# Performance work log

Measured on AMD Instinct MI355X. Metric: run time of the kernel, lower is better.

The kernel has to match this reference:

```python
import jax, jax.numpy as jnp
import numpy as np

N, T, D, H = 4, 2048, 1024, 16
DH = D // H
NEG = -1e20


def setup_inputs() -> dict:
    key = jax.random.key(0)
    ks = jax.random.split(key, 6)
    std = 1.0 / np.sqrt(D)
    return {
        "query": jax.random.normal(ks[0], (N, T, D), jnp.float32),
        "mask": jax.random.randint(ks[1], (N, T), 0, 2, jnp.int32),
        "Wq": jax.random.normal(ks[2], (D, D), jnp.float32) * std,
        "bq": jnp.zeros((D,), jnp.float32),
        "Wk": jax.random.normal(ks[3], (D, D), jnp.float32) * std,
        "bk": jnp.zeros((D,), jnp.float32),
        "Wv": jax.random.normal(ks[4], (D, D), jnp.float32) * std,
        "bv": jnp.zeros((D,), jnp.float32),
        "Wo": jax.random.normal(ks[5], (D, D), jnp.float32) * std,
        "bo": jnp.zeros((D,), jnp.float32),
    }


def _heads(x):
    # [N,T,D] -> [N,H,T,DH]
    n, t, _ = x.shape
    return x.reshape(n, t, H, DH).transpose(0, 2, 1, 3)


def reference(query, mask, Wq, bq, Wk, bk, Wv, bv, Wo, bo):
    scale = jnp.asarray(np.sqrt(DH), query.dtype)
    q = _heads(query @ Wq.T + bq)
    k = _heads(query @ Wk.T + bk)  # self-attention: key = value = query
    v = _heads(query @ Wv.T + bv)
    dot = jnp.einsum("nhtd,nhsd->nhts", q, k)  # [N,H,T,T_k]
    # 2D mask [N,T] aligns by name to the QUERY axis: (N,1,T,1)
    attn_mask = (mask == 0)[:, None, :, None]
    dot = jnp.where(attn_mask, jnp.asarray(NEG, dot.dtype), dot)
    # faithful to source: scale applied AFTER masked_fill, inside softmax arg
    attn = jax.nn.softmax(dot / scale, axis=-1)
    ctx = jnp.einsum("nhts,nhsd->nhtd", attn, v)  # [N,H,T,DH]
    ctx = ctx.transpose(0, 2, 1, 3).reshape(query.shape[0], query.shape[1], D)
    return ctx @ Wo.T + bo
```

## Files before the change

kernel.cpp:

```cpp
#include <hip/hip_runtime.h>

typedef _Float16 f16;
typedef __attribute__((ext_vector_type(8))) _Float16 half8;
typedef __attribute__((ext_vector_type(4))) _Float16 half4;
typedef __attribute__((ext_vector_type(4))) float f32x4;
typedef __attribute__((ext_vector_type(16))) float f32x16;

#define DEVINL __device__ __forceinline__

constexpr int NBATCH = 4, T = 2048, D = 1024, H = 16, DH = 64;
constexpr int M = NBATCH * T;
constexpr float SCL2 = 0.18033688011f;

DEVINL void async16(const f16* g, f16* l) {
  __builtin_amdgcn_global_load_lds(
      (__attribute__((address_space(1))) void*)(g),
      (__attribute__((address_space(3))) void*)(l), 16, 0, 0);
}

DEVINL unsigned pk2(float x, float y) {
  auto h = __builtin_amdgcn_cvt_pkrtz(x, y);
  return __builtin_bit_cast(unsigned, h);
}

union H8U {
  half8 h;
  unsigned u[4];
};

__global__ void cvt_all_kernel(const float* __restrict__ query,
                               const float* __restrict__ wq, const float* __restrict__ wk,
                               const float* __restrict__ wv, const float* __restrict__ wo,
                               f16* __restrict__ dst) {
  constexpr int NQ4 = M * D / 4;
  constexpr int NW4 = D * D / 4;
  constexpr int NT4 = NQ4 + 4 * NW4;
  const float* srcs[4] = {wq, wk, wv, wo};
  int i = blockIdx.x * blockDim.x + threadIdx.x;
  int stride = gridDim.x * blockDim.x;
  for (; i < NT4; i += stride) {
    const float* s;
    int off;
    if (i < NQ4) { s = query; off = i; }
    else {
      int j = i - NQ4;
      s = srcs[j >> 18];
      off = j & (NW4 - 1);
    }
    float4 v = reinterpret_cast<const float4*>(s)[off];
    half4 h = {(f16)v.x, (f16)v.y, (f16)v.z, (f16)v.w};
    reinterpret_cast<half4*>(dst)[i] = h;
  }
}

template<bool F32OUT>
DEVINL void gemm_body(const f16* __restrict__ A, const f16* __restrict__ W,
                      const float* __restrict__ bias, void* __restrict__ out,
                      f16* As, f16* Bs, long bm, long bn, float oscale) {
  constexpr int K = 1024, BK = 32, NCOL = 1024;
  const int tid = threadIdx.x;
  const int lane = tid & 63, wave = tid >> 6;
  const int wr = wave >> 1, wc = wave & 1;
  const int srow = tid >> 2, scol = (tid & 3) * 8;
  const f16* gA = A + (bm + srow) * (long)K + scol;
  const f16* gB = W + (bn + srow) * (long)K + scol;
  f16* lA = &As[srow * BK + scol];
  f16* lB = &Bs[srow * BK + scol];
  const int fr = lane & 15, fk = (lane >> 4) * 8;
  f32x4 acc[4][4] = {};

  for (int k0 = 0; k0 < K; k0 += BK) {
    async16(gA + k0, lA);
    async16(gA + k0 + 64 * K, lA + 64 * BK);
    async16(gB + k0, lB);
    async16(gB + k0 + 64 * K, lB + 64 * BK);
    __syncthreads();
    half8 af[4], bf[4];
#pragma unroll
    for (int m = 0; m < 4; ++m)
      af[m] = *(const half8*)&As[(wr * 64 + m * 16 + fr) * BK + fk];
#pragma unroll
    for (int n = 0; n < 4; ++n)
      bf[n] = *(const half8*)&Bs[(wc * 64 + n * 16 + fr) * BK + fk];
#pragma unroll
    for (int m = 0; m < 4; ++m)
#pragma unroll
      for (int n = 0; n < 4; ++n)
        acc[m][n] = __builtin_amdgcn_mfma_f32_16x16x32_f16(af[m], bf[n], acc[m][n], 0, 0, 0);
    __syncthreads();
  }
  const int rq = (lane >> 4) * 4;
#pragma unroll
  for (int m = 0; m < 4; ++m) {
    const long row = bm + wr * 64 + m * 16 + rq;
#pragma unroll
    for (int n = 0; n < 4; ++n) {
      const long col = bn + wc * 64 + n * 16 + fr;
      const float bb = bias[col];
#pragma unroll
      for (int r = 0; r < 4; ++r) {
        float v = (acc[m][n][r] + bb) * oscale;
        if (F32OUT) ((float*)out)[(row + r) * (long)NCOL + col] = v;
        else        ((f16*)out)[(row + r) * (long)NCOL + col] = (f16)v;
      }
    }
  }
}

__global__ __launch_bounds__(256) void gemm_qkv(const f16* __restrict__ A,
                                                const f16* __restrict__ Wall,
                                                const float* __restrict__ bq,
                                                const float* __restrict__ bk,
                                                const float* __restrict__ bv,
                                                f16* __restrict__ Qh,
                                                f16* __restrict__ Kh,
                                                f16* __restrict__ Vh) {
  __shared__ __align__(16) f16 As[128 * 32];
  __shared__ __align__(16) f16 Bs[128 * 32];
  const int z = blockIdx.z;
  const f16* W = Wall + (size_t)z * D * D;
  const float* bias = z == 0 ? bq : (z == 1 ? bk : bv);
  f16* out = z == 0 ? Qh : (z == 1 ? Kh : Vh);
  const float oscale = z == 0 ? SCL2 : 1.0f;
  gemm_body<false>(A, W, bias, (void*)out, As, Bs,
                   (long)blockIdx.y * 128, (long)blockIdx.x * 128, oscale);
}

__global__ __launch_bounds__(256) void gemm_out(const f16* __restrict__ A,
                                                const f16* __restrict__ W,
                                                const float* __restrict__ bias,
                                                float* __restrict__ out) {
  __shared__ __align__(16) f16 As[128 * 32];
  __shared__ __align__(16) f16 Bs[128 * 32];
  gemm_body<true>(A, W, bias, (void*)out, As, Bs,
                  (long)blockIdx.y * 128, (long)blockIdx.x * 128, 1.0f);
}

__global__ __launch_bounds__(256, 4) void attn_kernel(const f16* __restrict__ Qh,
                                                      const f16* __restrict__ Kh,
                                                      const f16* __restrict__ Vh,
                                                      const int* __restrict__ mask,
                                                      f16* __restrict__ Ch) {
  constexpr int NT = T / 64;
  constexpr int LDV = 72;
  __shared__ __align__(16) f16 smem[17408];
  f16* Ksb0 = smem;
  f16* Ksb1 = smem + 4096;
  f16* Vtb0 = smem + 8192;
  f16* Vtb1 = smem + 8192 + 4608;

  const int nh = blockIdx.y;
  const int bn = nh >> 4;
  const int bh = nh & 15;
  const int qt0 = blockIdx.x * 128;
  const int tid = threadIdx.x, lane = tid & 63, wave = tid >> 6;
  const int q = lane & 31, hi = lane >> 5;

  const long base = ((long)bn * T) * D + (long)bh * DH;
  const int qrow = qt0 + wave * 32 + q;

  const bool pm = mask[bn * T + qrow] != 0;
  half8 qf[4];
#pragma unroll
  for (int f = 0; f < 4; ++f) {
    qf[f] = *(const half8*)&Qh[base + (long)qrow * D + f * 16 + hi * 8];
    if (!pm) qf[f] = half8{};
  }

  f32x16 o0 = {}, o1 = {}, lacc = {};
  const f16 onev = (f16)1.0f;
  const half8 ones8 = {onev, onev, onev, onev, onev, onev, onev, onev};

  const int skey = tid >> 3;
  const int sc = tid & 7;
  const int kcol = ((sc ^ (skey & 7)) * 8);
  const f16* ksrc0 = Kh + base + (long)skey * D + kcol;
  const f16* ksrc1 = Kh + base + (long)(skey + 32) * D + kcol;

  const int vs = lane;
  const int vd = wave * 16;
  const f16* vsrc = Vh + base + (long)vs * D + vd;

  async16(ksrc0, Ksb0 + tid * 8);
  async16(ksrc1, Ksb0 + 2048 + tid * 8);
  half8 va = *(const half8*)(vsrc);
  half8 vb = *(const half8*)(vsrc + 8);
  {
#pragma unroll
    for (int j = 0; j < 8; ++j) Vtb0[(vd + j) * LDV + vs] = va[j];
#pragma unroll
    for (int j = 0; j < 8; ++j) Vtb0[(vd + 8 + j) * LDV + vs] = vb[j];
  }
  __syncthreads();

  for (int it = 0; it < NT; ++it) {
    const int cur = it & 1;
    f16* KsC = cur ? Ksb1 : Ksb0;
    f16* VtC = cur ? Vtb1 : Vtb0;
    f16* KsN = cur ? Ksb0 : Ksb1;
    f16* VtN = cur ? Vtb0 : Vtb1;

    if (it + 1 < NT) {
      const long koff = (long)(it + 1) * 64 * D;
      async16(ksrc0 + koff, KsN + tid * 8);
      async16(ksrc1 + koff, KsN + 2048 + tid * 8);
      va = *(const half8*)(vsrc + koff);
      vb = *(const half8*)(vsrc + koff + 8);
    }

    f32x16 s0 = {}, s1 = {};
    __builtin_amdgcn_s_setprio(1);
#pragma unroll
    for (int f = 0; f < 4; ++f) {
      const int ck = f * 2 + hi;
      half8 k0 = *(const half8*)&KsC[q * 64 + ((ck ^ (q & 7)) * 8)];
      half8 k1 = *(const half8*)&KsC[(32 + q) * 64 + ((ck ^ (q & 7)) * 8)];
      s0 = __builtin_amdgcn_mfma_f32_32x32x16_f16(k0, qf[f], s0, 0, 0, 0);
      s1 = __builtin_amdgcn_mfma_f32_32x32x16_f16(k1, qf[f], s1, 0, 0, 0);
    }
    __builtin_amdgcn_s_setprio(0);

#pragma unroll
    for (int r = 0; r < 16; ++r) {
      s0[r] = __builtin_amdgcn_exp2f(s0[r]);
      s1[r] = __builtin_amdgcn_exp2f(s1[r]);
    }

    half8 pf[4];
#pragma unroll
    for (int g = 0; g < 4; ++g) {
      float p0, p1, p2, p3, p4, p5, p6, p7;
      if (g == 0) { p0=s0[0];p1=s0[1];p2=s0[2];p3=s0[3];p4=s0[4];p5=s0[5];p6=s0[6];p7=s0[7]; }
      else if (g == 1) { p0=s0[8];p1=s0[9];p2=s0[10];p3=s0[11];p4=s0[12];p5=s0[13];p6=s0[14];p7=s0[15]; }
      else if (g == 2) { p0=s1[0];p1=s1[1];p2=s1[2];p3=s1[3];p4=s1[4];p5=s1[5];p6=s1[6];p7=s1[7]; }
      else { p0=s1[8];p1=s1[9];p2=s1[10];p3=s1[11];p4=s1[12];p5=s1[13];p6=s1[14];p7=s1[15]; }
      unsigned A0 = pk2(p0, p1), A1 = pk2(p2, p3);
      unsigned B0 = pk2(p4, p5), B1 = pk2(p6, p7);
      asm("v_permlane32_swap_b32 %0, %1" : "+v"(A0), "+v"(B0));
      asm("v_permlane32_swap_b32 %0, %1" : "+v"(A1), "+v"(B1));
      H8U u;
      u.u[0] = A0;
      u.u[1] = A1;
      u.u[2] = B0;
      u.u[3] = B1;
      pf[g] = u.h;
    }

    __builtin_amdgcn_s_setprio(1);
#pragma unroll
    for (int kc = 0; kc < 4; ++kc) {
      half8 v0f = *(const half8*)&VtC[q * LDV + kc * 16 + hi * 8];
      half8 v1f = *(const half8*)&VtC[(32 + q) * LDV + kc * 16 + hi * 8];
      o0 = __builtin_amdgcn_mfma_f32_32x32x16_f16(v0f, pf[kc], o0, 0, 0, 0);
      o1 = __builtin_amdgcn_mfma_f32_32x32x16_f16(v1f, pf[kc], o1, 0, 0, 0);
      lacc = __builtin_amdgcn_mfma_f32_32x32x16_f16(ones8, pf[kc], lacc, 0, 0, 0);
    }
    __builtin_amdgcn_s_setprio(0);

    if (it + 1 < NT) {
#pragma unroll
      for (int j = 0; j < 8; ++j) VtN[(vd + j) * LDV + vs] = va[j];
#pragma unroll
      for (int j = 0; j < 8; ++j) VtN[(vd + 8 + j) * LDV + vs] = vb[j];
    }
    __syncthreads();
  }

  constexpr int EPL = 72;
  const float rl = 1.0f / lacc[0];
  f16* ep = smem + wave * 2304;
#pragma unroll
  for (int r = 0; r < 16; r += 2) {
    const int dd = (r & 3) + 8 * (r >> 2) + 4 * hi;
    *(unsigned*)&ep[q * EPL + dd]      = pk2(o0[r] * rl, o0[r + 1] * rl);
    *(unsigned*)&ep[q * EPL + 32 + dd] = pk2(o1[r] * rl, o1[r + 1] * rl);
  }
  asm volatile("s_waitcnt lgkmcnt(0)" ::: "memory");
  const int rr = lane >> 1, cw = lane & 1;
  const long orow = base + (long)(qt0 + wave * 32 + rr) * D + cw * 32;
#pragma unroll
  for (int c2 = 0; c2 < 4; ++c2) {
    half8 val = *(const half8*)&ep[rr * EPL + cw * 32 + c2 * 8];
    *(half8*)&Ch[orow + c2 * 8] = val;
  }
}

extern "C" void kernel_launch(void* const* d_in, const int* in_sizes, int n_in,
                              void* d_out, int out_size, void* d_ws, size_t ws_size,
                              hipStream_t stream) {
  const float* query = (const float*)d_in[0];
  const int*   mask  = (const int*)d_in[1];
  const float* Wq = (const float*)d_in[2];
  const float* bq = (const float*)d_in[3];
  const float* Wk = (const float*)d_in[4];
  const float* bk = (const float*)d_in[5];
  const float* Wv = (const float*)d_in[6];
  const float* bv = (const float*)d_in[7];
  const float* Wo = (const float*)d_in[8];
  const float* bo = (const float*)d_in[9];

  char* ws = (char*)d_ws;
  const size_t MD = (size_t)M * D;
  f16* Xh = (f16*)ws;
  f16* Wh = (f16*)(ws + (16u << 20));
  f16* Qh = (f16*)(ws + (24u << 20));
  f16 *KhP, *VhP;
  const size_t need = (24u << 20) + 3 * MD * sizeof(f16);
  if (ws_size >= need) {
    KhP = Qh + MD; VhP = KhP + MD;
  } else {
    KhP = (f16*)d_out; VhP = KhP + MD;
  }
  f16* Ch = Xh;

  cvt_all_kernel<<<dim3(2048), dim3(256), 0, stream>>>(query, Wq, Wk, Wv, Wo, Xh);

  gemm_qkv<<<dim3(8, 64, 3), dim3(256), 0, stream>>>(Xh, Wh, bq, bk, bv, Qh, KhP, VhP);

  attn_kernel<<<dim3(T / 128, NBATCH * H), dim3(256), 0, stream>>>(Qh, KhP, VhP, mask, Ch);

  gemm_out<<<dim3(8, 64), dim3(256), 0, stream>>>(Ch, Wh + 3 * (size_t)D * D, bo, (float*)d_out);
}
```

Before: 199.8 us.

## Software-pipeline attention loop and compute row sums with packed dot instead of MFMA

Restructures the attention inner loop into a two-stage software pipeline. The PV MFMAs for the previous tile now run alongside the QK MFMAs of the current tile, and K/V tiles are prefetched two iterations ahead using double-buffered registers and LDS. The ones-vector MFMA that accumulated the softmax denominator is replaced by fdot2 sums on packed fp16 probabilities, followed by a cross-half shuffle. This removes a third of the PV-stage MFMAs and hides exp/pack latency behind matrix work, at the cost of more live registers and a more complex buffer rotation.

Measured after the change: 360.3 us. +80.3%, slower.

```diff
diff --git a/kernel.cpp b/kernel.cpp
--- a/kernel.cpp
+++ b/kernel.cpp
@@ -3,6 +3,7 @@
 typedef _Float16 f16;
 typedef __attribute__((ext_vector_type(8))) _Float16 half8;
 typedef __attribute__((ext_vector_type(4))) _Float16 half4;
+typedef __attribute__((ext_vector_type(2))) __fp16 fp16x2;
 typedef __attribute__((ext_vector_type(4))) float f32x4;
 typedef __attribute__((ext_vector_type(16))) float f32x16;
 
@@ -22,6 +23,8 @@
   auto h = __builtin_amdgcn_cvt_pkrtz(x, y);
   return __builtin_bit_cast(unsigned, h);
 }
+
+DEVINL fp16x2 u2h(unsigned u) { return __builtin_bit_cast(fp16x2, u); }
 
 union H8U {
   half8 h;
@@ -167,9 +170,9 @@
     if (!pm) qf[f] = half8{};
   }
 
-  f32x16 o0 = {}, o1 = {}, lacc = {};
-  const f16 onev = (f16)1.0f;
-  const half8 ones8 = {onev, onev, onev, onev, onev, onev, onev, onev};
+  f32x16 o0 = {}, o1 = {};
+  float lsum = 0.0f;
+  const fp16x2 one2 = {(__fp16)1.0f, (__fp16)1.0f};
 
   const int skey = tid >> 3;
   const int sc = tid & 7;
@@ -183,91 +186,111 @@
 
   async16(ksrc0, Ksb0 + tid * 8);
   async16(ksrc1, Ksb0 + 2048 + tid * 8);
-  half8 va = *(const half8*)(vsrc);
-  half8 vb = *(const half8*)(vsrc + 8);
+  async16(ksrc0 + 64 * D, Ksb1 + tid * 8);
+  async16(ksrc1 + 64 * D, Ksb1 + 2048 + tid * 8);
+  half8 vA0 = *(const half8*)(vsrc);
+  half8 vA1 = *(const half8*)(vsrc + 8);
+  half8 vB0 = *(const half8*)(vsrc + 64 * D);
+  half8 vB1 = *(const half8*)(vsrc + 64 * D + 8);
   {
 #pragma unroll
-    for (int j = 0; j < 8; ++j) Vtb0[(vd + j) * LDV + vs] = va[j];
-#pragma unroll
-    for (int j = 0; j < 8; ++j) Vtb0[(vd + 8 + j) * LDV + vs] = vb[j];
+    for (int j = 0; j < 8; ++j) Vtb0[(vd + j) * LDV + vs] = vA0[j];
+#pragma unroll
+    for (int j = 0; j < 8; ++j) Vtb0[(vd + 8 + j) * LDV + vs] = vA1[j];
   }
   __syncthreads();
 
-  for (int it = 0; it < NT; ++it) {
-    const int cur = it & 1;
-    f16* KsC = cur ? Ksb1 : Ksb0;
-    f16* VtC = cur ? Vtb1 : Vtb0;
-    f16* KsN = cur ? Ksb0 : Ksb1;
-    f16* VtN = cur ? Vtb0 : Vtb1;
-
-    if (it + 1 < NT) {
-      const long koff = (long)(it + 1) * 64 * D;
-      async16(ksrc0 + koff, KsN + tid * 8);
-      async16(ksrc1 + koff, KsN + 2048 + tid * 8);
-      va = *(const half8*)(vsrc + koff);
-      vb = *(const half8*)(vsrc + koff + 8);
-    }
-
-    f32x16 s0 = {}, s1 = {};
+  half8 pfA[4], pfB[4];
+
+#define ATTN_BODY(T_, PFC, PFN, KB, VP, W0, W1, L0, L1)                         \
+  {                                                                             \
+    const int t_ = (T_);                                                        \
+    f32x16 s0 = {}, s1 = {};                                                    \
+    __builtin_amdgcn_s_setprio(1);                                              \
+    _Pragma("unroll")                                                           \
+    for (int f = 0; f < 4; ++f) {                                               \
+      const int ck = f * 2 + hi;                                                \
+      half8 k0 = *(const half8*)&KB[q * 64 + ((ck ^ (q & 7)) * 8)];             \
+      half8 k1 = *(const half8*)&KB[(32 + q) * 64 + ((ck ^ (q & 7)) * 8)];      \
+      s0 = __builtin_amdgcn_mfma_f32_32x32x16_f16(k0, qf[f], s0, 0, 0, 0);      \
+      s1 = __builtin_amdgcn_mfma_f32_32x32x16_f16(k1, qf[f], s1, 0, 0, 0);      \
+    }                                                                           \
+    if (t_ > 0) {                                                               \
+      _Pragma("unroll")                                                         \
+      for (int kc = 0; kc < 4; ++kc) {                                          \
+        half8 v0f = *(const half8*)&VP[q * LDV + kc * 16 + hi * 8];             \
+        half8 v1f = *(const half8*)&VP[(32 + q) * LDV + kc * 16 + hi * 8];      \
+        o0 = __builtin_amdgcn_mfma_f32_32x32x16_f16(v0f, PFC[kc], o0, 0, 0, 0); \
+        o1 = __builtin_amdgcn_mfma_f32_32x32x16_f16(v1f, PFC[kc], o1, 0, 0, 0); \
+      }                                                                         \
+    }                                                                           \
+    __builtin_amdgcn_s_setprio(0);                                              \
+    _Pragma("unroll")                                                           \
+    for (int r = 0; r < 16; ++r) {                                              \
+      s0[r] = __builtin_amdgcn_exp2f(s0[r]);                                    \
+      s1[r] = __builtin_amdgcn_exp2f(s1[r]);                                    \
+    }                                                                           \
+    _Pragma("unroll")                                                           \
+    for (int g = 0; g < 4; ++g) {                                               \
+      float p0, p1, p2, p3, p4, p5, p6, p7;                                     \
+      if (g == 0) { p0=s0[0];p1=s0[1];p2=s0[2];p3=s0[3];p4=s0[4];p5=s0[5];p6=s0[6];p7=s0[7]; } \
+      else if (g == 1) { p0=s0[8];p1=s0[9];p2=s0[10];p3=s0[11];p4=s0[12];p5=s0[13];p6=s0[14];p7=s0[15]; } \
+      else if (g == 2) { p0=s1[0];p1=s1[1];p2=s1[2];p3=s1[3];p4=s1[4];p5=s1[5];p6=s1[6];p7=s1[7]; } \
+      else { p0=s1[8];p1=s1[9];p2=s1[10];p3=s1[11];p4=s1[12];p5=s1[13];p6=s1[14];p7=s1[15]; } \
+      unsigned A0 = pk2(p0, p1), A1 = pk2(p2, p3);                              \
+      unsigned B0 = pk2(p4, p5), B1 = pk2(p6, p7);                              \
+      float sgs = __builtin_amdgcn_fdot2(u2h(A0), one2, 0.0f, false);           \
+      sgs = __builtin_amdgcn_fdot2(u2h(A1), one2, sgs, false);                  \
+      sgs = __builtin_amdgcn_fdot2(u2h(B0), one2, sgs, false);                  \
+      sgs = __builtin_amdgcn_fdot2(u2h(B1), one2, sgs, false);                  \
+      lsum += sgs;                                                              \
+      asm("v_permlane32_swap_b32 %0, %1" : "+v"(A0), "+v"(B0));                 \
+      asm("v_permlane32_swap_b32 %0, %1" : "+v"(A1), "+v"(B1));                 \
+      H8U u;                                                                    \
+      u.u[0] = A0; u.u[1] = A1; u.u[2] = B0; u.u[3] = B1;                       \
+      PFN[g] = u.h;                                                             \
+    }                                                                           \
+    __syncthreads();                                                            \
+    if (t_ + 2 < NT) {                                                          \
+      const long koff = (long)(t_ + 2) * 64 * D;                                \
+      async16(ksrc0 + koff, KB + tid * 8);                                      \
+      async16(ksrc1 + koff, KB + 2048 + tid * 8);                               \
+    }                                                                           \
+    if (t_ + 1 < NT) {                                                          \
+      _Pragma("unroll")                                                         \
+      for (int j = 0; j < 8; ++j) VP[(vd + j) * LDV + vs] = W0[j];              \
+      _Pragma("unroll")                                                         \
+      for (int j = 0; j < 8; ++j) VP[(vd + 8 + j) * LDV + vs] = W1[j];          \
+    }                                                                           \
+    if (t_ + 2 < NT) {                                                          \
+      const long koff2 = (long)(t_ + 2) * 64 * D;                               \
+      L0 = *(const half8*)(vsrc + koff2);                                       \
+      L1 = *(const half8*)(vsrc + koff2 + 8);                                   \
+    }                                                                           \
+  }
+
+  for (int t2 = 0; t2 < NT; t2 += 2) {
+    ATTN_BODY(t2, pfA, pfB, Ksb0, Vtb1, vB0, vB1, vA0, vA1)
+    ATTN_BODY(t2 + 1, pfB, pfA, Ksb1, Vtb0, vA0, vA1, vB0, vB1)
+  }
+#undef ATTN_BODY
+
+  {
     __builtin_amdgcn_s_setprio(1);
 #pragma unroll
-    for (int f = 0; f < 4; ++f) {
-      const int ck = f * 2 + hi;
-      half8 k0 = *(const half8*)&KsC[q * 64 + ((ck ^ (q & 7)) * 8)];
-      half8 k1 = *(const half8*)&KsC[(32 + q) * 64 + ((ck ^ (q & 7)) * 8)];
-      s0 = __builtin_amdgcn_mfma_f32_32x32x16_f16(k0, qf[f], s0, 0, 0, 0);
-      s1 = __builtin_amdgcn_mfma_f32_32x32x16_f16(k1, qf[f], s1, 0, 0, 0);
+    for (int kc = 0; kc < 4; ++kc) {
+      half8 v0f = *(const half8*)&Vtb1[q * LDV + kc * 16 + hi * 8];
+      half8 v1f = *(const half8*)&Vtb1[(32 + q) * LDV + kc * 16 + hi * 8];
+      o0 = __builtin_amdgcn_mfma_f32_32x32x16_f16(v0f, pfA[kc], o0, 0, 0, 0);
+      o1 = __builtin_amdgcn_mfma_f32_32x32x16_f16(v1f, pfA[kc], o1, 0, 0, 0);
     }
     __builtin_amdgcn_s_setprio(0);
-
-#pragma unroll
-    for (int r = 0; r < 16; ++r) {
-      s0[r] = __builtin_amdgcn_exp2f(s0[r]);
-      s1[r] = __builtin_amdgcn_exp2f(s1[r]);
-    }
-
-    half8 pf[4];
-#pragma unroll
-    for (int g = 0; g < 4; ++g) {
-      float p0, p1, p2, p3, p4, p5, p6, p7;
-      if (g == 0) { p0=s0[0];p1=s0[1];p2=s0[2];p3=s0[3];p4=s0[4];p5=s0[5];p6=s0[6];p7=s0[7]; }
-      else if (g == 1) { p0=s0[8];p1=s0[9];p2=s0[10];p3=s0[11];p4=s0[12];p5=s0[13];p6=s0[14];p7=s0[15]; }
-      else if (g == 2) { p0=s1[0];p1=s1[1];p2=s1[2];p3=s1[3];p4=s1[4];p5=s1[5];p6=s1[6];p7=s1[7]; }
-      else { p0=s1[8];p1=s1[9];p2=s1[10];p3=s1[11];p4=s1[12];p5=s1[13];p6=s1[14];p7=s1[15]; }
-      unsigned A0 = pk2(p0, p1), A1 = pk2(p2, p3);
-      unsigned B0 = pk2(p4, p5), B1 = pk2(p6, p7);
-      asm("v_permlane32_swap_b32 %0, %1" : "+v"(A0), "+v"(B0));
-      asm("v_permlane32_swap_b32 %0, %1" : "+v"(A1), "+v"(B1));
-      H8U u;
-      u.u[0] = A0;
-      u.u[1] = A1;
-      u.u[2] = B0;
-      u.u[3] = B1;
-      pf[g] = u.h;
-    }
-
-    __builtin_amdgcn_s_setprio(1);
-#pragma unroll
-    for (int kc = 0; kc < 4; ++kc) {
-      half8 v0f = *(const half8*)&VtC[q * LDV + kc * 16 + hi * 8];
-      half8 v1f = *(const half8*)&VtC[(32 + q) * LDV + kc * 16 + hi * 8];
-      o0 = __builtin_amdgcn_mfma_f32_32x32x16_f16(v0f, pf[kc], o0, 0, 0, 0);
-      o1 = __builtin_amdgcn_mfma_f32_32x32x16_f16(v1f, pf[kc], o1, 0, 0, 0);
-      lacc = __builtin_amdgcn_mfma_f32_32x32x16_f16(ones8, pf[kc], lacc, 0, 0, 0);
-    }
-    __builtin_amdgcn_s_setprio(0);
-
-    if (it + 1 < NT) {
-#pragma unroll
-      for (int j = 0; j < 8; ++j) VtN[(vd + j) * LDV + vs] = va[j];
-#pragma unroll
-      for (int j = 0; j < 8; ++j) VtN[(vd + 8 + j) * LDV + vs] = vb[j];
-    }
-    __syncthreads();
-  }
-
+  }
+  __syncthreads();
+
+  float lrow = lsum + __shfl_xor(lsum, 32);
   constexpr int EPL = 72;
-  const float rl = 1.0f / lacc[0];
+  const float rl = 1.0f / lrow;
   f16* ep = smem + wave * 2304;
 #pragma unroll
   for (int r = 0; r < 16; r += 2) {
```
